# Kernel optimization log

Hardware: AMD Instinct MI355X
Metric: run time of the kernel (lower is better)

Reference implementation:

```python
import jax, jax.numpy as jnp
import numpy as np
from jax import lax

HEADS = 8
SHIFTS = 4
WS = 8          # window_size
C = 192         # channels
MID = C // 2    # 96
EPS = 1e-5      # BatchNorm eps (inference mode, running stats)


def _shift_mask(out_c, in_c):
    """ShiftConv2d0 mask: each channel group only sees one shifted tap of the 3x3 kernel."""
    m = np.zeros((out_c, in_c, 3, 3), np.float32)
    g = in_c // 5
    m[:, 0 * g:1 * g, 1, 2] = 1.0
    m[:, 1 * g:2 * g, 1, 0] = 1.0
    m[:, 2 * g:3 * g, 2, 1] = 1.0
    m[:, 3 * g:4 * g, 0, 1] = 1.0
    m[:, 4 * g:, 1, 1] = 1.0
    return jnp.asarray(m)


def _shift_conv(x, w, b, mask):
    y = lax.conv_general_dilated(x, w * mask, (1, 1), ((1, 1), (1, 1)),
                                 dimension_numbers=('NCHW', 'OIHW', 'NCHW'))
    return y + b[None, :, None, None]


def _bn(x, gamma, beta, mean, var):
    scale = gamma / jnp.sqrt(var + EPS)
    return (x - mean[None, :, None, None]) * scale[None, :, None, None] + beta[None, :, None, None]


def _to_windows(t):
    # b (head c) (h dh) (w dw) -> (b h w) head (dh dw) c
    b, c, H, W = t.shape
    cph = c // HEADS
    hh, ww = H // WS, W // WS
    t = t.reshape(b, HEADS, cph, hh, WS, ww, WS)
    t = t.transpose(0, 3, 5, 1, 4, 6, 2)  # b hh ww head dh dw c
    return t.reshape(b * hh * ww, HEADS, WS * WS, cph)


def _from_windows(t, b, hh, ww):
    # (b h w) head (dh dw) c -> b (head c) (h dh) (w dw)
    cph = t.shape[-1]
    t = t.reshape(b, hh, ww, HEADS, WS, WS, cph)
    t = t.transpose(0, 3, 6, 1, 4, 2, 5)  # b head c hh dh ww dw
    return t.reshape(b, HEADS * cph, hh * WS, ww * WS)


def setup_inputs() -> dict:
    key = jax.random.key(0)
    ks = jax.random.split(key, 24)
    d = {"x": jax.random.normal(ks[0], (4, C, 256, 256), jnp.float32)}
    i = 1
    for name in ("theta", "phi", "g"):
        d[f"w_{name}"] = jax.random.normal(ks[i], (MID, C, 3, 3), jnp.float32) * 0.05; i += 1
        d[f"b_{name}"] = jax.random.normal(ks[i], (MID,), jnp.float32) * 0.05; i += 1
        d[f"gamma_{name}"] = jax.random.uniform(ks[i], (MID,), jnp.float32) + 0.5; i += 1
        d[f"beta_{name}"] = jax.random.normal(ks[i], (MID,), jnp.float32) * 0.1; i += 1
        d[f"mean_{name}"] = jax.random.normal(ks[i], (MID,), jnp.float32) * 0.1; i += 1
        d[f"var_{name}"] = jax.random.uniform(ks[i], (MID,), jnp.float32) + 0.5; i += 1
    d["w_out"] = jax.random.normal(ks[i], (C, MID, 3, 3), jnp.float32) * 0.05; i += 1
    d["b_out"] = jax.random.normal(ks[i], (C,), jnp.float32) * 0.05
    return d


def reference(x, w_theta, b_theta, gamma_theta, beta_theta, mean_theta, var_theta,
              w_phi, b_phi, gamma_phi, beta_phi, mean_phi, var_phi,
              w_g, b_g, gamma_g, beta_g, mean_g, var_g,
              w_out, b_out):
    mask_in = _shift_mask(MID, C)
    mask_out = _shift_mask(C, MID)
    S = SHIFTS
    xp = jnp.pad(x, ((0, 0), (0, 0), (S, S), (S, S)))
    b, _, H, W = xp.shape
    hh, ww = H // WS, W // WS

    theta = _bn(_shift_conv(xp, w_theta, b_theta, mask_in), gamma_theta, beta_theta, mean_theta, var_theta)
    phi = _bn(_shift_conv(xp, w_phi, b_phi, mask_in), gamma_phi, beta_phi, mean_phi, var_phi)
    g = _bn(_shift_conv(xp, w_g, b_g, mask_in), gamma_g, beta_g, mean_g, var_g)

    q = _to_windows(theta)  # [BW, head, WS*WS, c]
    k = _to_windows(phi)
    v = _to_windows(g)

    sim = jnp.einsum('nhqc,nhkc->nhqk', q, k)  # no 1/sqrt(d) scaling in original
    attn = jax.nn.softmax(sim, axis=-1)
    out = jnp.einsum('nhqk,nhkc->nhqc', attn, v)

    out = _from_windows(out, b, hh, ww)
    out = _shift_conv(out, w_out, b_out, mask_out)
    return out[:, :, S:-S, S:-S]
```

## Files before the change

kernel.cpp:

```cpp
#include <hip/hip_runtime.h>
#include <math.h>

typedef unsigned int  uint32;
typedef unsigned short u16;
typedef __attribute__((ext_vector_type(8))) short short8;
typedef __attribute__((ext_vector_type(4))) float f32x4;
typedef __attribute__((ext_vector_type(16))) float f32x16;
typedef __attribute__((ext_vector_type(4))) unsigned int u32x4;

#define NB     4
#define CIN    192
#define MID_C  96
#define OC3    288
#define HH     33
#define NWIN   (NB*HH*HH)
#define PADW   264
#define IMGW   256

__device__ __forceinline__ u16 f2bf(float f) {
    union { float f; uint32 u; } v; v.f = f;
    uint32 u = v.u;
    return (u16)((u + 0x7fffu + ((u >> 16) & 1u)) >> 16);
}
__device__ __forceinline__ float bfu_to_f(u16 h) {
    union { uint32 u; float f; } v; v.u = ((uint32)h) << 16; return v.f;
}
__device__ __forceinline__ float bf_lo(uint32 u) {
    union { uint32 u; float f; } v; v.u = (u << 16); return v.f;
}
__device__ __forceinline__ float bf_hi(uint32 u) {
    union { uint32 u; float f; } v; v.u = (u & 0xffff0000u); return v.f;
}
__device__ __forceinline__ float hi_trunc_f(uint32 u) {
    union { uint32 u; float f; } v; v.u = (u & 0xffff0000u); return v.f;
}
__device__ __forceinline__ uint32 cvtpk_bf16(float a, float b) {
    uint32 r;
    asm("v_cvt_pk_bf16_f32 %0, %1, %2" : "=v"(r) : "v"(a), "v"(b));
    return r;
}

struct PrepArgs {
    const float* w[3];
    const float* b[3];
    const float* gamma[3];
    const float* beta[3];
    const float* mean[3];
    const float* var[3];
    const float* w_out;
    const float* b_out;
    u16*   Wbf;
    u16*   WbfO;
    float* beff;
    float* bout;
};

__global__ __launch_bounds__(256) void prep_kernel(PrepArgs a) {
    int i = blockIdx.x * 256 + threadIdx.x;
    const int khs[5] = {1,1,2,0,1};
    const int kws[5] = {2,0,1,1,1};
    if (i < 288*192) {
        int oc = i / 192, c = i % 192;
        int t = oc / 96, och = oc % 96;
        int grp = (c < 152) ? (c / 38) : 4;
        float scale = a.gamma[t][och] / sqrtf(a.var[t][och] + 1e-5f);
        float v = a.w[t][(och*192 + c)*9 + khs[grp]*3 + kws[grp]] * scale;
        a.Wbf[i] = f2bf(v);
    } else if (i < 288*192 + 192*96) {
        int j = i - 288*192;
        int o = j / 96, c = j % 96;
        int grp = (c < 76) ? (c / 19) : 4;
        a.WbfO[j] = f2bf(a.w_out[(o*96 + c)*9 + khs[grp]*3 + kws[grp]]);
    } else if (i < 288*192 + 192*96 + 480) {
        int j = i - (288*192 + 192*96);
        if (j < 288) {
            int t = j / 96, och = j % 96;
            float scale = a.gamma[t][och] / sqrtf(a.var[t][och] + 1e-5f);
            a.beff[j] = a.beta[t][och] + (a.b[t][och] - a.mean[t][och]) * scale;
        } else {
            a.bout[j - 288] = a.b_out[j - 288];
        }
    }
}

__global__ __launch_bounds__(256, 3) void qkv_attn_kernel(
    const float* __restrict__ x,
    const u16*   __restrict__ Wbf,
    const float* __restrict__ beff,
    u16*         __restrict__ attn_sp)
{
    __shared__ uint32 xs32[3200];
    __shared__ __align__(16) u16 qkv[3][64][100];
    __shared__ int shoff[192];

    int blk = blockIdx.x;
    int b   = blk / (HH*HH);
    int rem = blk % (HH*HH);
    int wy  = rem / HH;
    int wx  = rem % HH;
    int tid = threadIdx.x;
    int lane = tid & 63;
    int nt   = __builtin_amdgcn_readfirstlane(tid >> 6);
    int l15  = lane & 15;
    int quad = lane >> 4;

    if (tid < 192) {
        int c = tid;
        int grp = (c < 152) ? (c / 38) : 4;
        int dy = 0, dx = 0;
        if (grp == 0) dx = 1; else if (grp == 1) dx = -1;
        else if (grp == 2) dy = 1; else if (grp == 3) dy = -1;
        shoff[c] = dy*10 + dx;
    }

    int px    = nt*16 + l15;
    int pbase = (1 + (px >> 3))*10 + 1 + (px & 7);

    int gy0 = wy*8 - 1;
    int gx0 = wx*8 - 1;
    const bool border = (wy == 0) || (wy == 32) || (wx == 0) || (wx == 32);

    int   goff[13];
    float emul[13];
    #pragma unroll
    for (int k = 0; k < 13; ++k) {
        int p   = tid + (k << 8);
        int pp  = (p < 3200) ? p : 0;
        int cc  = pp / 100;
        int pos = pp % 100;
        int r   = pos / 10, col = pos % 10;
        int gy  = gy0 + r, gx = gx0 + col;
        bool valid = (gy >= 4) && (gy < 260) && (gx >= 4) && (gx < 260);
        int cgy = min(max(gy, 4), 259);
        int cgx = min(max(gx, 4), 259);
        goff[k] = cc*65536 + (cgy - 4)*256 + (cgx - 4);
        emul[k] = valid ? 1.f : 0.f;
    }

    const float* xb = x + (size_t)(b*CIN)*65536;

    f32x4 acc[18];
    #pragma unroll
    for (int mt = 0; mt < 18; ++mt) acc[mt] = (f32x4){0.f, 0.f, 0.f, 0.f};

    float bufA[13], bufB[13];

    auto LOADX = [&](float* buf, int chunk) {
        const float* bp = xb + chunk*(32*65536);
        #pragma unroll
        for (int k = 0; k < 12; ++k) buf[k] = bp[goff[k]];
        if (tid < 128) buf[12] = bp[goff[12]];
    };

    auto STOREX = [&](float* buf) {
        if (border) {
            #pragma unroll
            for (int k = 0; k < 12; ++k) buf[k] *= emul[k];
            if (tid < 128) buf[12] *= emul[12];
        }
        #pragma unroll
        for (int kk = 0; kk < 6; ++kk) {
            float v0 = buf[2*kk], v1 = buf[2*kk+1];
            uint32 ph = cvtpk_bf16(v0, v1);
            uint32 pl = cvtpk_bf16(v0 - bf_lo(ph), v1 - bf_hi(ph));
            xs32[tid + (2*kk)*256]   = (ph & 0xffffu) | (pl << 16);
            xs32[tid + (2*kk+1)*256] = (ph >> 16)     | (pl & 0xffff0000u);
        }
        if (tid < 128) {
            float v = buf[12];
            uint32 ph = cvtpk_bf16(v, v);
            uint32 pl = cvtpk_bf16(v - bf_lo(ph), 0.f);
            xs32[tid + 12*256] = (ph & 0xffffu) | (pl << 16);
        }
    };

    auto COMPUTE = [&](int chunk) {
        short8 bh, bl;
        #pragma unroll
        for (int j = 0; j < 8; ++j) {
            int cc = quad*8 + j;
            uint32 w = xs32[cc*100 + pbase + shoff[chunk*32 + cc]];
            bh[j] = (short)(u16)(w & 0xffffu);
            bl[j] = (short)(u16)(w >> 16);
        }
        const u16* Abase = Wbf + l15*192 + chunk*32 + quad*8;
        #pragma unroll
        for (int mt = 0; mt < 18; ++mt) {
            short8 af = *(const short8*)(Abase + mt*16*192);
            acc[mt] = __builtin_amdgcn_mfma_f32_16x16x32_bf16(af, bh, acc[mt], 0, 0, 0);
            acc[mt] = __builtin_amdgcn_mfma_f32_16x16x32_bf16(af, bl, acc[mt], 0, 0, 0);
        }
    };

    LOADX(bufA, 0);
    #pragma unroll
    for (int cpair = 0; cpair < 3; ++cpair) {
        const int c0 = cpair*2;
        LOADX(bufB, c0 + 1);
        __syncthreads();
        STOREX(bufA);
        __syncthreads();
        COMPUTE(c0);
        if (cpair < 2) LOADX(bufA, c0 + 2);
        __syncthreads();
        STOREX(bufB);
        __syncthreads();
        COMPUTE(c0 + 1);
    }

    #pragma unroll
    for (int mt = 0; mt < 18; ++mt) {
        #pragma unroll
        for (int r = 0; r < 4; ++r) {
            int oc  = mt*16 + quad*4 + r;
            int t   = oc / 96;
            int och = oc % 96;
            qkv[t][px][och] = f2bf(acc[mt][r] + beff[oc]);
        }
    }
    __syncthreads();

    {
        const int l31 = lane & 31;
        const int hl  = lane >> 5;
        const int vcl = (l31 < 12) ? l31 : 11;

        #pragma unroll 1
        for (int hrep = 0; hrep < 2; ++hrep) {
            const int head  = nt*2 + hrep;
            const int cbase = head*12 + hl*8;

            auto ldf = [&](const u16* p) -> short8 {
                const uint32* w = (const uint32*)p;
                union { u32x4 u; short8 s; } t_;
                t_.u[0] = w[0];
                t_.u[1] = w[1];
                t_.u[2] = hl ? 0u : w[2];
                t_.u[3] = hl ? 0u : w[3];
                return t_.s;
            };
            short8 kf0 = ldf(&qkv[1][l31][cbase]);
            short8 kf1 = ldf(&qkv[1][32 + l31][cbase]);
            short8 qf0 = ldf(&qkv[0][l31][cbase]);
            short8 qf1 = ldf(&qkv[0][32 + l31][cbase]);

            f32x16 z;
            #pragma unroll
            for (int i = 0; i < 16; ++i) z[i] = 0.f;

            f32x16 sA0 = __builtin_amdgcn_mfma_f32_32x32x16_bf16(kf0, qf0, z, 0, 0, 0);
            f32x16 sB0 = __builtin_amdgcn_mfma_f32_32x32x16_bf16(kf1, qf0, z, 0, 0, 0);
            f32x16 sA1 = __builtin_amdgcn_mfma_f32_32x32x16_bf16(kf0, qf1, z, 0, 0, 0);
            f32x16 sB1 = __builtin_amdgcn_mfma_f32_32x32x16_bf16(kf1, qf1, z, 0, 0, 0);

            auto softmax_col = [&](f32x16& SA, f32x16& SB) {
                float m0 = fmaxf(SA[0], SB[0]);
                float m1 = fmaxf(SA[1], SB[1]);
                float m2 = fmaxf(SA[2], SB[2]);
                float m3 = fmaxf(SA[3], SB[3]);
                #pragma unroll
                for (int i = 4; i < 16; i += 4) {
                    m0 = fmaxf(m0, fmaxf(SA[i+0], SB[i+0]));
                    m1 = fmaxf(m1, fmaxf(SA[i+1], SB[i+1]));
                    m2 = fmaxf(m2, fmaxf(SA[i+2], SB[i+2]));
                    m3 = fmaxf(m3, fmaxf(SA[i+3], SB[i+3]));
                }
                float mx = fmaxf(fmaxf(m0, m1), fmaxf(m2, m3));
                mx = fmaxf(mx, __shfl_xor(mx, 32));
                float s0 = 0.f, s1 = 0.f, s2 = 0.f, s3 = 0.f;
                #pragma unroll
                for (int i = 0; i < 16; i += 4) {
                    SA[i+0] = __expf(SA[i+0] - mx); s0 += SA[i+0];
                    SA[i+1] = __expf(SA[i+1] - mx); s1 += SA[i+1];
                    SA[i+2] = __expf(SA[i+2] - mx); s2 += SA[i+2];
                    SA[i+3] = __expf(SA[i+3] - mx); s3 += SA[i+3];
                    SB[i+0] = __expf(SB[i+0] - mx); s0 += SB[i+0];
                    SB[i+1] = __expf(SB[i+1] - mx); s1 += SB[i+1];
                    SB[i+2] = __expf(SB[i+2] - mx); s2 += SB[i+2];
                    SB[i+3] = __expf(SB[i+3] - mx); s3 += SB[i+3];
                }
                float sum = (s0 + s1) + (s2 + s3);
                sum += __shfl_xor(sum, 32);
                float inv = 1.f / sum;
                #pragma unroll
                for (int i = 0; i < 16; ++i) { SA[i] *= inv; SB[i] *= inv; }
            };
            softmax_col(sA0, sB0);
            softmax_col(sA1, sB1);

            f32x16 o0 = z, o1 = z;
            #pragma unroll
            for (int ks = 0; ks < 4; ++ks) {
                short8 vf;
                #pragma unroll
                for (int j = 0; j < 8; ++j)
                    vf[j] = (short)qkv[2][ks*16 + hl*8 + j][head*12 + vcl];

                auto pv_step = [&](const f32x16& S, f32x16& O) {
                    const int base = (ks & 1) * 8;
                    float p0 = S[base+0], p1 = S[base+1], p2 = S[base+2], p3 = S[base+3];
                    float p4 = S[base+4], p5 = S[base+5], p6 = S[base+6], p7 = S[base+7];
                    uint32 u0 = __float_as_uint(p0), u1 = __float_as_uint(p1);
                    uint32 u2 = __float_as_uint(p2), u3 = __float_as_uint(p3);
                    uint32 u4 = __float_as_uint(p4), u5 = __float_as_uint(p5);
                    uint32 u6 = __float_as_uint(p6), u7 = __float_as_uint(p7);
                    uint32 h0_01 = (u1 & 0xffff0000u) | (u0 >> 16);
                    uint32 h0_23 = (u3 & 0xffff0000u) | (u2 >> 16);
                    uint32 h1_01 = (u5 & 0xffff0000u) | (u4 >> 16);
                    uint32 h1_23 = (u7 & 0xffff0000u) | (u6 >> 16);
                    uint32 l0_01 = (uint32)f2bf(p0 - hi_trunc_f(u0)) | ((uint32)f2bf(p1 - hi_trunc_f(u1)) << 16);
                    uint32 l0_23 = (uint32)f2bf(p2 - hi_trunc_f(u2)) | ((uint32)f2bf(p3 - hi_trunc_f(u3)) << 16);
                    uint32 l1_01 = (uint32)f2bf(p4 - hi_trunc_f(u4)) | ((uint32)f2bf(p5 - hi_trunc_f(u5)) << 16);
                    uint32 l1_23 = (uint32)f2bf(p6 - hi_trunc_f(u6)) | ((uint32)f2bf(p7 - hi_trunc_f(u7)) << 16);
                    uint32 kh01 = hl ? h1_01 : h0_01, kh23 = hl ? h1_23 : h0_23;
                    uint32 sh01 = hl ? h0_01 : h1_01, sh23 = hl ? h0_23 : h1_23;
                    uint32 kl01 = hl ? l1_01 : l0_01, kl23 = hl ? l1_23 : l0_23;
                    uint32 sl01 = hl ? l0_01 : l1_01, sl23 = hl ? l0_23 : l1_23;
                    uint32 rh01 = __shfl_xor(sh01, 32);
                    uint32 rh23 = __shfl_xor(sh23, 32);
                    uint32 rl01 = __shfl_xor(sl01, 32);
                    uint32 rl23 = __shfl_xor(sl23, 32);
                    union { u32x4 u; short8 s; } fh, fl;
                    fh.u[0] = hl ? rh01 : kh01;  fh.u[1] = hl ? rh23 : kh23;
                    fh.u[2] = hl ? kh01 : rh01;  fh.u[3] = hl ? kh23 : rh23;
                    fl.u[0] = hl ? rl01 : kl01;  fl.u[1] = hl ? rl23 : kl23;
                    fl.u[2] = hl ? kl01 : rl01;  fl.u[3] = hl ? kl23 : rl23;
                    O = __builtin_amdgcn_mfma_f32_32x32x16_bf16(fh.s, vf, O, 0, 0, 0);
                    O = __builtin_amdgcn_mfma_f32_32x32x16_bf16(fl.s, vf, O, 0, 0, 0);
                };
                if (ks < 2) { pv_step(sA0, o0); pv_step(sA1, o1); }
                else        { pv_step(sB0, o0); pv_step(sB1, o1); }
            }

            if (l31 < 12) {
                u16* ob = attn_sp + (((b*MID_C + head*12 + l31)*PADW + wy*8)*PADW + wx*8);
                #pragma unroll
                for (int r = 0; r < 16; r += 2) {
                    const int c0  = (r & 3) + 8*(r >> 2);
                    const int pyw = c0 >> 3;
                    const int pxw = (c0 & 7) + 4*hl;
                    *(uint32*)&ob[pyw*PADW + pxw]     = cvtpk_bf16(o0[r], o0[r+1]);
                    *(uint32*)&ob[(pyw+4)*PADW + pxw] = cvtpk_bf16(o1[r], o1[r+1]);
                }
            }
        }
    }
}

__global__ __launch_bounds__(256, 3) void outconv_kernel(
    const u16*   __restrict__ sp,
    const u16*   __restrict__ WbfO,
    const float* __restrict__ bout,
    float*       __restrict__ out)
{
    __shared__ u16 xs[96][10][20];
    __shared__ int shoff[96];

    int blk = blockIdx.x;
    int b   = blk >> 9;
    int rem = blk & 511;
    int ty  = rem >> 4;
    int tx  = rem & 15;
    int tid = threadIdx.x;
    int lane = tid & 63;
    int ntw  = __builtin_amdgcn_readfirstlane(tid >> 6);
    int l15  = lane & 15;
    int quad = lane >> 4;

    if (tid < 96) {
        int c = tid;
        int grp = (c < 76) ? (c / 19) : 4;
        int dy = 0, dx = 0;
        if (grp == 0) dx = 1; else if (grp == 1) dx = -1;
        else if (grp == 2) dy = 1; else if (grp == 3) dy = -1;
        shoff[c] = dy*20 + dx;
    }

    int py0  = ty*8 + 3;
    int px0m = tx*16 + 2;

    {
        const uint32* spu = (const uint32*)sp;
        uint32* xw = (uint32*)&xs[0][0][0];
        int c0 = (tid >> 5) * 12;
        int u  = tid & 31;
        #pragma unroll
        for (int j = 0; j < 4; ++j) {
            int uu = u + 32*j;
            if (uu < 100) {
                int r = uu / 10, w = uu % 10;
                int rb = (((py0 + r)*PADW + px0m) >> 1) + w;
                #pragma unroll
                for (int m = 0; m < 12; ++m) {
                    int c = c0 + m;
                    xw[c*100 + r*10 + w] = spu[(b*MID_C + c)*34848 + rb];
                }
            }
        }
    }
    __syncthreads();

    const u16* xf = &xs[0][0][0];

    f32x4 acc[3][8];
    #pragma unroll
    for (int mt = 0; mt < 3; ++mt)
        #pragma unroll
        for (int np = 0; np < 8; ++np) acc[mt][np] = (f32x4){0.f, 0.f, 0.f, 0.f};

    #pragma unroll
    for (int ks = 0; ks < 3; ++ks) {
        short8 bfr[8];
        #pragma unroll
        for (int np = 0; np < 8; ++np) {
            int pb = (1 + np)*20 + 2 + l15;
            #pragma unroll
            for (int j = 0; j < 8; ++j) {
                int cc = ks*32 + quad*8 + j;
                bfr[np][j] = (short)xf[cc*200 + pb + shoff[cc]];
            }
        }
        const u16* Ab = WbfO + (ntw*48)*96 + l15*96 + ks*32 + quad*8;
        #pragma unroll
        for (int mt = 0; mt < 3; ++mt) {
            short8 af = *(const short8*)(Ab + mt*16*96);
            #pragma unroll
            for (int np = 0; np < 8; ++np)
                acc[mt][np] = __builtin_amdgcn_mfma_f32_16x16x32_bf16(af, bfr[np], acc[mt][np], 0, 0, 0);
        }
    }

    int oxb = tx*16 + l15;
    #pragma unroll
    for (int mt = 0; mt < 3; ++mt) {
        #pragma unroll
        for (int rr = 0; rr < 4; ++rr) {
            int oc = ntw*48 + mt*16 + quad*4 + rr;
            float bo = bout[oc];
            #pragma unroll
            for (int np = 0; np < 8; ++np) {
                int oy = ty*8 + np;
                out[((b*CIN + oc)*IMGW + oy)*IMGW + oxb] = acc[mt][np][rr] + bo;
            }
        }
    }
}

extern "C" void kernel_launch(void* const* d_in, const int* in_sizes, int n_in,
                              void* d_out, int out_size, void* d_ws, size_t ws_size,
                              hipStream_t stream) {
    const float* x = (const float*)d_in[0];

    PrepArgs a;
    for (int t = 0; t < 3; ++t) {
        a.w[t]     = (const float*)d_in[1 + 6*t];
        a.b[t]     = (const float*)d_in[2 + 6*t];
        a.gamma[t] = (const float*)d_in[3 + 6*t];
        a.beta[t]  = (const float*)d_in[4 + 6*t];
        a.mean[t]  = (const float*)d_in[5 + 6*t];
        a.var[t]   = (const float*)d_in[6 + 6*t];
    }
    a.w_out = (const float*)d_in[19];
    a.b_out = (const float*)d_in[20];

    char* ws = (char*)d_ws;
    u16*   Wbf     = (u16*)ws;
    u16*   WbfO    = (u16*)(ws + 110592);
    float* beff    = (float*)(ws + 147456);
    float* bout    = (float*)(ws + 148608);
    u16*   attn_sp = (u16*)(ws + 149504);

    a.Wbf = Wbf; a.WbfO = WbfO; a.beff = beff; a.bout = bout;

    const int prep_items = 288*192 + 192*96 + 480;
    prep_kernel<<<(prep_items + 255)/256, 256, 0, stream>>>(a);
    qkv_attn_kernel<<<NWIN, 256, 0, stream>>>(x, Wbf, beff, attn_sp);
    outconv_kernel<<<NB*32*16, 256, 0, stream>>>(attn_sp, WbfO, bout, (float*)d_out);
}
```

Before: 726.1 us.

## Transpose shared-memory tiles to channel-minor with pre-applied shifts for vector B-fragment loads

```diff
diff --git a/kernel.cpp b/kernel.cpp
--- a/kernel.cpp
+++ b/kernel.cpp
@@ -21,9 +21,6 @@
     union { float f; uint32 u; } v; v.f = f;
     uint32 u = v.u;
     return (u16)((u + 0x7fffu + ((u >> 16) & 1u)) >> 16);
-}
-__device__ __forceinline__ float bfu_to_f(u16 h) {
-    union { uint32 u; float f; } v; v.u = ((uint32)h) << 16; return v.f;
 }
 __device__ __forceinline__ float bf_lo(uint32 u) {
     union { uint32 u; float f; } v; v.u = (u << 16); return v.f;
@@ -89,8 +86,8 @@
     const float* __restrict__ beff,
     u16*         __restrict__ attn_sp)
 {
-    __shared__ uint32 xs32[3200];
-    __shared__ __align__(16) u16 qkv[3][64][100];
+    __shared__ __align__(16) uint32 xs_t[100*36];
+    __shared__ __align__(16) u16 qkv[3][64][98];
     __shared__ int shoff[192];
 
     int blk = blockIdx.x;
@@ -120,20 +117,20 @@
     int gx0 = wx*8 - 1;
     const bool border = (wy == 0) || (wy == 32) || (wx == 0) || (wx == 32);
 
+    const int cs  = tid >> 3;
+    const int pb8 = tid & 7;
     int   goff[13];
     float emul[13];
     #pragma unroll
     for (int k = 0; k < 13; ++k) {
-        int p   = tid + (k << 8);
-        int pp  = (p < 3200) ? p : 0;
-        int cc  = pp / 100;
-        int pos = pp % 100;
-        int r   = pos / 10, col = pos % 10;
+        int pos = pb8 + 8*k;
+        int pp  = (pos < 100) ? pos : 99;
+        int r   = pp / 10, col = pp % 10;
         int gy  = gy0 + r, gx = gx0 + col;
         bool valid = (gy >= 4) && (gy < 260) && (gx >= 4) && (gx < 260);
         int cgy = min(max(gy, 4), 259);
         int cgx = min(max(gx, 4), 259);
-        goff[k] = cc*65536 + (cgy - 4)*256 + (cgx - 4);
+        goff[k] = cs*65536 + (cgy - 4)*256 + (cgx - 4);
         emul[k] = valid ? 1.f : 0.f;
     }
 
@@ -149,39 +146,48 @@
         const float* bp = xb + chunk*(32*65536);
         #pragma unroll
         for (int k = 0; k < 12; ++k) buf[k] = bp[goff[k]];
-        if (tid < 128) buf[12] = bp[goff[12]];
+        if (pb8 < 4) buf[12] = bp[goff[12]];
     };
 
-    auto STOREX = [&](float* buf) {
+    auto STOREX = [&](float* buf, int chunk) {
+        int sh = shoff[chunk*32 + cs];
         if (border) {
             #pragma unroll
             for (int k = 0; k < 12; ++k) buf[k] *= emul[k];
-            if (tid < 128) buf[12] *= emul[12];
+            if (pb8 < 4) buf[12] *= emul[12];
         }
         #pragma unroll
         for (int kk = 0; kk < 6; ++kk) {
             float v0 = buf[2*kk], v1 = buf[2*kk+1];
             uint32 ph = cvtpk_bf16(v0, v1);
             uint32 pl = cvtpk_bf16(v0 - bf_lo(ph), v1 - bf_hi(ph));
-            xs32[tid + (2*kk)*256]   = (ph & 0xffffu) | (pl << 16);
-            xs32[tid + (2*kk+1)*256] = (ph >> 16)     | (pl & 0xffff0000u);
-        }
-        if (tid < 128) {
+            uint32 w0 = (ph & 0xffffu) | (pl << 16);
+            uint32 w1 = (ph >> 16)     | (pl & 0xffff0000u);
+            int d0 = pb8 + 16*kk - sh;
+            int d1 = pb8 + 16*kk + 8 - sh;
+            if ((unsigned)d0 < 100u) xs_t[d0*36 + cs] = w0;
+            if ((unsigned)d1 < 100u) xs_t[d1*36 + cs] = w1;
+        }
+        if (pb8 < 4) {
             float v = buf[12];
             uint32 ph = cvtpk_bf16(v, v);
             uint32 pl = cvtpk_bf16(v - bf_lo(ph), 0.f);
-            xs32[tid + 12*256] = (ph & 0xffffu) | (pl << 16);
+            int d = pb8 + 96 - sh;
+            if ((unsigned)d < 100u) xs_t[d*36 + cs] = (ph & 0xffffu) | (pl << 16);
         }
     };
 
+    const u32x4* bp128 = (const u32x4*)&xs_t[pbase*36 + quad*8];
+
     auto COMPUTE = [&](int chunk) {
+        u32x4 w0 = bp128[0], w1 = bp128[1];
         short8 bh, bl;
         #pragma unroll
-        for (int j = 0; j < 8; ++j) {
-            int cc = quad*8 + j;
-            uint32 w = xs32[cc*100 + pbase + shoff[chunk*32 + cc]];
-            bh[j] = (short)(u16)(w & 0xffffu);
-            bl[j] = (short)(u16)(w >> 16);
+        for (int j = 0; j < 4; ++j) {
+            bh[j]   = (short)(u16)(w0[j] & 0xffffu);
+            bl[j]   = (short)(u16)(w0[j] >> 16);
+            bh[4+j] = (short)(u16)(w1[j] & 0xffffu);
+            bl[4+j] = (short)(u16)(w1[j] >> 16);
         }
         const u16* Abase = Wbf + l15*192 + chunk*32 + quad*8;
         #pragma unroll
@@ -198,12 +204,12 @@
         const int c0 = cpair*2;
         LOADX(bufB, c0 + 1);
         __syncthreads();
-        STOREX(bufA);
+        STOREX(bufA, c0);
         __syncthreads();
         COMPUTE(c0);
         if (cpair < 2) LOADX(bufA, c0 + 2);
         __syncthreads();
-        STOREX(bufB);
+        STOREX(bufB, c0 + 1);
         __syncthreads();
         COMPUTE(c0 + 1);
     }
@@ -225,7 +231,7 @@
         const int hl  = lane >> 5;
         const int vcl = (l31 < 12) ? l31 : 11;
 
-        #pragma unroll 1
+        #pragma unroll
         for (int hrep = 0; hrep < 2; ++hrep) {
             const int head  = nt*2 + hrep;
             const int cbase = head*12 + hl*8;
@@ -353,8 +359,7 @@
     const float* __restrict__ bout,
     float*       __restrict__ out)
 {
-    __shared__ u16 xs[96][10][20];
-    __shared__ int shoff[96];
+    __shared__ __align__(16) u16 xs_t[200][104];
 
     int blk = blockIdx.x;
     int b   = blk >> 9;
@@ -367,41 +372,45 @@
     int l15  = lane & 15;
     int quad = lane >> 4;
 
-    if (tid < 96) {
-        int c = tid;
+    int py0  = ty*8 + 3;
+    int px0m = tx*16 + 2;
+
+    int c0 = (tid >> 5) * 12;
+    int shm[12];
+    #pragma unroll
+    for (int m = 0; m < 12; ++m) {
+        int c = c0 + m;
         int grp = (c < 76) ? (c / 19) : 4;
         int dy = 0, dx = 0;
         if (grp == 0) dx = 1; else if (grp == 1) dx = -1;
         else if (grp == 2) dy = 1; else if (grp == 3) dy = -1;
-        shoff[c] = dy*20 + dx;
-    }
-
-    int py0  = ty*8 + 3;
-    int px0m = tx*16 + 2;
+        shm[m] = dy*20 + dx;
+    }
 
     {
         const uint32* spu = (const uint32*)sp;
-        uint32* xw = (uint32*)&xs[0][0][0];
-        int c0 = (tid >> 5) * 12;
-        int u  = tid & 31;
+        int u = tid & 31;
         #pragma unroll
         for (int j = 0; j < 4; ++j) {
             int uu = u + 32*j;
             if (uu < 100) {
-                int r = uu / 10, w = uu % 10;
-                int rb = (((py0 + r)*PADW + px0m) >> 1) + w;
+                int r = uu / 10, w10 = uu % 10;
+                int rb = (((py0 + r)*PADW + px0m) >> 1) + w10;
+                int pos0 = r*20 + 2*w10;
                 #pragma unroll
                 for (int m = 0; m < 12; ++m) {
                     int c = c0 + m;
-                    xw[c*100 + r*10 + w] = spu[(b*MID_C + c)*34848 + rb];
+                    uint32 wv = spu[(b*MID_C + c)*34848 + rb];
+                    int d0 = pos0 - shm[m];
+                    int d1 = pos0 + 1 - shm[m];
+                    if ((unsigned)d0 < 200u) xs_t[d0][c] = (u16)(wv & 0xffffu);
+                    if ((unsigned)d1 < 200u) xs_t[d1][c] = (u16)(wv >> 16);
                 }
             }
         }
     }
     __syncthreads();
 
-    const u16* xf = &xs[0][0][0];
-
     f32x4 acc[3][8];
     #pragma unroll
     for (int mt = 0; mt < 3; ++mt)
@@ -414,11 +423,7 @@
         #pragma unroll
         for (int np = 0; np < 8; ++np) {
             int pb = (1 + np)*20 + 2 + l15;
-            #pragma unroll
-            for (int j = 0; j < 8; ++j) {
-                int cc = ks*32 + quad*8 + j;
-                bfr[np][j] = (short)xf[cc*200 + pb + shoff[cc]];
-            }
+            bfr[np] = *(const short8*)&xs_t[pb][ks*32 + quad*8];
         }
         const u16* Ab = WbfO + (ntw*48)*96 + l15*96 + ks*32 + quad*8;
         #pragma unroll
```

Measured after the change: 754.4 us. 1.04x slower.
